# Performance work log

Measured on AMD Instinct MI355X. Metric: run time of the kernel, lower is better.

## Reference

```python
import jax, jax.numpy as jnp
import numpy as np

H = 128        # hidden_channels
NU = 200000    # num users
NM = 80000     # num movies
E = 2_000_000  # num 'rates' edges
EL = 500_000   # num supervision (edge_label) edges
FD = 512       # movie_feat_dim


def setup_inputs() -> dict:
    key = jax.random.key(0)
    ks = jax.random.split(key, 24)
    def w(k, shape):
        # Glorot-ish init for linear weights
        scale = 1.0 / np.sqrt(shape[0])
        return jax.random.uniform(k, shape, jnp.float32, -scale, scale)
    inp = {
        "movie_feats": jax.random.normal(ks[0], (NM, FD), jnp.float32),
        "user_init": jnp.zeros((H,), jnp.float32),  # requires_grad=False param
        "edge_src": jax.random.randint(ks[1], (E,), 0, NU),   # user index per rates-edge
        "edge_dst": jax.random.randint(ks[2], (E,), 0, NM),   # movie index per rates-edge
        "lbl_user": jax.random.randint(ks[3], (EL,), 0, NU),
        "lbl_movie": jax.random.randint(ks[4], (EL,), 0, NM),
        "n_users": NU,
        # movie_lin
        "Wm": w(ks[5], (FD, H)), "bm": jnp.zeros((H,), jnp.float32),
        # conv1, relation user->movie ('rates'): lin_l (neighbor, with bias), lin_r (root, no bias)
        "Wl1_um": w(ks[6], (H, H)), "bl1_um": jnp.zeros((H,), jnp.float32), "Wr1_um": w(ks[7], (H, H)),
        # conv1, relation movie->user ('rev_rates')
        "Wl1_mu": w(ks[8], (H, H)), "bl1_mu": jnp.zeros((H,), jnp.float32), "Wr1_mu": w(ks[9], (H, H)),
        # conv2, user->movie
        "Wl2_um": w(ks[10], (H, H)), "bl2_um": jnp.zeros((H,), jnp.float32), "Wr2_um": w(ks[11], (H, H)),
        # conv2, movie->user
        "Wl2_mu": w(ks[12], (H, H)), "bl2_mu": jnp.zeros((H,), jnp.float32), "Wr2_mu": w(ks[13], (H, H)),
    }
    return inp


def _mean_agg(x_src, src, dst, num_dst):
    # gather source features along edges, scatter-mean into destination nodes
    msgs = x_src[src]                                             # [E, H]
    s = jax.ops.segment_sum(msgs, dst, num_segments=num_dst)      # [num_dst, H]
    cnt = jax.ops.segment_sum(jnp.ones(src.shape, x_src.dtype), dst, num_segments=num_dst)
    return s / jnp.maximum(cnt, 1.0)[:, None]


def _sage(x_src, x_dst, src, dst, Wl, bl, Wr):
    # PyG SAGEConv (aggr='mean'): lin_l(mean_j x_j) + lin_r(x_i); bias only on lin_l
    agg = _mean_agg(x_src, src, dst, x_dst.shape[0])
    return agg @ Wl + bl + x_dst @ Wr


def reference(movie_feats, user_init, edge_src, edge_dst, lbl_user, lbl_movie, n_users,
              Wm, bm,
              Wl1_um, bl1_um, Wr1_um, Wl1_mu, bl1_mu, Wr1_mu,
              Wl2_um, bl2_um, Wr2_um, Wl2_mu, bl2_mu, Wr2_mu):
    # initial node embeddings
    user_x = jnp.tile(user_init[None, :], (n_users, 1))           # [NU, H]
    movie_x = movie_feats @ Wm + bm                               # [NM, H]

    # conv1 (hetero): movie aggregates users via 'rates', user aggregates movies via reverse
    movie_h = _sage(user_x, movie_x, edge_src, edge_dst, Wl1_um, bl1_um, Wr1_um)
    user_h = _sage(movie_x, user_x, edge_dst, edge_src, Wl1_mu, bl1_mu, Wr1_mu)
    movie_h = jax.nn.relu(movie_h)   # dropout p=0.0 -> identity
    user_h = jax.nn.relu(user_h)

    # conv2
    movie_o = _sage(user_h, movie_h, edge_src, edge_dst, Wl2_um, bl2_um, Wr2_um)
    user_o = _sage(movie_h, user_h, edge_dst, edge_src, Wl2_mu, bl2_mu, Wr2_mu)

    # edge-wise dot product on supervision edges
    return (user_o[lbl_user] * movie_o[lbl_movie]).sum(axis=-1)   # [EL]
```

## Files before the change

### kernel.cpp

```cpp
#include <hip/hip_runtime.h>

#define H 128
#define SU 36
#define SM 64

typedef unsigned short u16;
typedef __attribute__((ext_vector_type(8))) short s16x8;
typedef __attribute__((ext_vector_type(4))) float f32x4;

static __device__ __forceinline__ float4 f4zero() { return make_float4(0.f, 0.f, 0.f, 0.f); }
static __device__ __forceinline__ void f4add(float4& a, const float4& b) {
  a.x += b.x; a.y += b.y; a.z += b.z; a.w += b.w;
}
static __device__ __forceinline__ float bf2f(u16 v) {
  return __uint_as_float(((unsigned int)v) << 16);
}
static __device__ __forceinline__ u16 f2bf(float f) {
  unsigned int u = __float_as_uint(f);
  return (u16)((u + 0x7FFF + ((u >> 16) & 1)) >> 16);
}
static __device__ __forceinline__ float4 load4(const u16* p) {
  ushort4 v = *(const ushort4*)p;
  return make_float4(bf2f(v.x), bf2f(v.y), bf2f(v.z), bf2f(v.w));
}
static __device__ __forceinline__ void store4(u16* p, float4 v) {
  ushort4 o;
  o.x = f2bf(v.x); o.y = f2bf(v.y); o.z = f2bf(v.z); o.w = f2bf(v.w);
  *(ushort4*)p = o;
}
static __device__ __forceinline__ void store1(u16* p, float v) { *p = f2bf(v); }

static __device__ __forceinline__ s16x8 frag_from(const u16* p, float) {
  return __builtin_bit_cast(s16x8, *(const uint4*)p);
}
static __device__ __forceinline__ s16x8 frag_from(const float* p, float s) {
  float4 a = *(const float4*)p;
  float4 b = *(const float4*)(p + 4);
  s16x8 v;
  v[0] = (short)f2bf(a.x * s); v[1] = (short)f2bf(a.y * s);
  v[2] = (short)f2bf(a.z * s); v[3] = (short)f2bf(a.w * s);
  v[4] = (short)f2bf(b.x * s); v[5] = (short)f2bf(b.y * s);
  v[6] = (short)f2bf(b.z * s); v[7] = (short)f2bf(b.w * s);
  return v;
}
static __device__ __forceinline__ f32x4 mfma16(s16x8 a, s16x8 b, f32x4 c) {
  return __builtin_amdgcn_mfma_f32_16x16x32_bf16(a, b, c, 0, 0, 0);
}

__global__ void fillfs_u(const int* __restrict__ src, const int* __restrict__ dst,
                         int* __restrict__ cnt, int* __restrict__ adj,
                         float inv, int rbase, int E) {
  int r = (blockIdx.x & 7) + rbase;
  int e = (blockIdx.x >> 3) * blockDim.x + threadIdx.x;
  if (e >= E) return;
  int s = __builtin_nontemporal_load(&src[e]);
  int reg = (int)((float)s * inv);
  if (reg > 15) reg = 15;
  if (reg != r) return;
  int d = __builtin_nontemporal_load(&dst[e]);
  int slot = atomicAdd(&cnt[s], 1);
  if (slot < SU) adj[(size_t)s * SU + slot] = d;
}

__global__ void fillfs_m(const int* __restrict__ src, const int* __restrict__ dst,
                         int* __restrict__ cnt, int* __restrict__ adj,
                         float inv, int E) {
  int r = blockIdx.x & 7;
  int e = (blockIdx.x >> 3) * blockDim.x + threadIdx.x;
  if (e >= E) return;
  int d = __builtin_nontemporal_load(&dst[e]);
  int reg = (int)((float)d * inv);
  if (reg > 7) reg = 7;
  if (reg != r) return;
  int s = __builtin_nontemporal_load(&src[e]);
  int slot = atomicAdd(&cnt[d], 1);
  if (slot < SM) adj[(size_t)d * SM + slot] = s;
}

__global__ void uvec_kernel(const float* __restrict__ u, const float* __restrict__ W1,
                            const float* __restrict__ W2, float* __restrict__ outv1,
                            float* __restrict__ outv2) {
  int h = threadIdx.x;
  float a1 = 0.f, a2 = 0.f;
  for (int k = 0; k < H; k++) {
    float uk = u[k];
    a1 += uk * W1[k * H + h];
    a2 += uk * W2[k * H + h];
  }
  outv1[h] = a1;
  outv2[h] = a2;
}

__global__ void pack_w_all(const float* __restrict__ Wm, const float* __restrict__ Wa,
                           const float* __restrict__ Wb, const float* __restrict__ Wc,
                           const float* __restrict__ Wd, const float* __restrict__ We,
                           const float* __restrict__ Wf, u16* __restrict__ out) {
  int gid = blockIdx.x * blockDim.x + threadIdx.x;
  int chunk = gid >> 11;
  int e = gid & 2047;
  const float* W;
  int kbase = 0;
  if (chunk < 4) { W = Wm; kbase = chunk * 128; }
  else if (chunk == 4) W = Wa;
  else if (chunk == 5) W = Wb;
  else if (chunk == 6) W = Wc;
  else if (chunk == 7) W = Wd;
  else if (chunk == 8) W = We;
  else W = Wf;
  int lane = e & 63;
  int k0 = kbase + ((e >> 6) & 3) * 32 + (lane >> 4) * 8;
  int n = (e >> 8) * 16 + (lane & 15);
  u16 tmp[8];
#pragma unroll
  for (int j = 0; j < 8; j++) tmp[j] = f2bf(W[(size_t)(k0 + j) * H + n]);
  *(uint4*)(out + (size_t)gid * 8) = *(const uint4*)tmp;
}

template <typename TXb>
__global__ __launch_bounds__(256, 4) void mfma_gemm(
    u16* __restrict__ out,
    const u16* __restrict__ Xa, const u16* __restrict__ WpA,
    const TXb* __restrict__ Xb, const u16* __restrict__ WpB, int Kb,
    const float* __restrict__ bl, const float* __restrict__ vec,
    const int* __restrict__ cnt_ind, int relu, int N) {
  int tid = threadIdx.x;
  int lane = tid & 63;
  int wv = tid >> 6;
  int m16 = lane & 15;
  int quad = lane >> 4;
  int rowW = blockIdx.x * 128 + wv * 32;

  f32x4 acc[2][8];
#pragma unroll
  for (int rt = 0; rt < 2; rt++)
#pragma unroll
    for (int ct = 0; ct < 8; ct++) acc[rt][ct] = (f32x4){0.f, 0.f, 0.f, 0.f};

  int ra0 = rowW + m16;      if (ra0 > N - 1) ra0 = N - 1;
  int ra1 = rowW + 16 + m16; if (ra1 > N - 1) ra1 = N - 1;

  if (Xa) {
    const u16* wp = WpA + (size_t)lane * 8;
#pragma unroll
    for (int ks4 = 0; ks4 < 4; ks4++) {
      int ko = ks4 * 32 + quad * 8;
      s16x8 a0 = frag_from(Xa + (size_t)ra0 * 128 + ko, 1.f);
      s16x8 a1 = frag_from(Xa + (size_t)ra1 * 128 + ko, 1.f);
#pragma unroll
      for (int ct = 0; ct < 8; ct++) {
        s16x8 b = __builtin_bit_cast(
            s16x8, *(const uint4*)(wp + ct * 2048 + ks4 * 512));
        acc[0][ct] = mfma16(a0, b, acc[0][ct]);
        acc[1][ct] = mfma16(a1, b, acc[1][ct]);
      }
    }
  }

  if (Xb) {
    for (int kc = 0; kc < Kb; kc += 128) {
      const u16* wp = WpB + (size_t)(kc >> 7) * 16384 + (size_t)lane * 8;
#pragma unroll
      for (int ks4 = 0; ks4 < 4; ks4++) {
        int ko = ks4 * 32 + quad * 8;
        s16x8 a0 = frag_from(Xb + (size_t)ra0 * Kb + kc + ko, 1.f);
        s16x8 a1 = frag_from(Xb + (size_t)ra1 * Kb + kc + ko, 1.f);
#pragma unroll
        for (int ct = 0; ct < 8; ct++) {
          s16x8 b = __builtin_bit_cast(
              s16x8, *(const uint4*)(wp + ct * 2048 + ks4 * 512));
          acc[0][ct] = mfma16(a0, b, acc[0][ct]);
          acc[1][ct] = mfma16(a1, b, acc[1][ct]);
        }
      }
    }
  }

  float bcol[8], vcol[8];
#pragma unroll
  for (int ct = 0; ct < 8; ct++) {
    int col = ct * 16 + m16;
    bcol[ct] = bl ? bl[col] : 0.f;
    vcol[ct] = vec ? vec[col] : 0.f;
  }
#pragma unroll
  for (int rt = 0; rt < 2; rt++) {
#pragma unroll
    for (int rg = 0; rg < 4; rg++) {
      int r = rowW + rt * 16 + quad * 4 + rg;
      if (r >= N) continue;
      float ind = 0.f;
      if (vec) ind = (cnt_ind ? (cnt_ind[r] > 0 ? 1.f : 0.f) : 1.f);
#pragma unroll
      for (int ct = 0; ct < 8; ct++) {
        float o = acc[rt][ct][rg] + bcol[ct] + ind * vcol[ct];
        if (relu) o = fmaxf(o, 0.f);
        store1(out + (size_t)r * H + ct * 16 + m16, o);
      }
    }
  }
}

__global__ __launch_bounds__(256) void agg_bf(
    u16* __restrict__ outb, const u16* __restrict__ xsrc,
    const int* __restrict__ adj, int stride,
    const int* __restrict__ cnt, const float* __restrict__ bl,
    const float* __restrict__ vec, int mode, int N) {
  int wid = (blockIdx.x * blockDim.x + threadIdx.x) >> 6;
  if (wid >= N) return;
  int lane = threadIdx.x & 63;
  int c4 = lane & 31;
  int slot = lane >> 5;
  size_t s0 = (size_t)wid * stride;
  int c = cnt[wid];
  int cl = c > stride ? stride : c;
  float4 acc = f4zero();
  int i = slot;
  while (i + 6 < cl) {
    int n0 = adj[s0 + i];
    int n1 = adj[s0 + i + 2];
    int n2 = adj[s0 + i + 4];
    int n3 = adj[s0 + i + 6];
    float4 v0 = load4(xsrc + (size_t)n0 * H + c4 * 4);
    float4 v1 = load4(xsrc + (size_t)n1 * H + c4 * 4);
    float4 v2 = load4(xsrc + (size_t)n2 * H + c4 * 4);
    float4 v3 = load4(xsrc + (size_t)n3 * H + c4 * 4);
    f4add(acc, v0);
    f4add(acc, v1);
    f4add(acc, v2);
    f4add(acc, v3);
    i += 8;
  }
  while (i < cl) {
    int n0 = adj[s0 + i];
    float4 v0 = load4(xsrc + (size_t)n0 * H + c4 * 4);
    f4add(acc, v0);
    i += 2;
  }
  acc.x += __shfl_xor(acc.x, 32);
  acc.y += __shfl_xor(acc.y, 32);
  acc.z += __shfl_xor(acc.z, 32);
  acc.w += __shfl_xor(acc.w, 32);
  if (slot == 0) {
    float s = 1.f / (float)(c > 1 ? c : 1);
    u16* op = outb + (size_t)wid * H + c4 * 4;
    if (mode == 1) {
      float4 o = load4(op);
      o.x += s * acc.x; o.y += s * acc.y; o.z += s * acc.z; o.w += s * acc.w;
      store4(op, o);
    } else if (mode == 2) {
      float4 b4 = *(const float4*)(bl + c4 * 4);
      float4 r4 = *(const float4*)(vec + c4 * 4);
      float4 o;
      o.x = fmaxf(s * acc.x + b4.x + r4.x, 0.f);
      o.y = fmaxf(s * acc.y + b4.y + r4.y, 0.f);
      o.z = fmaxf(s * acc.z + b4.z + r4.z, 0.f);
      o.w = fmaxf(s * acc.w + b4.w + r4.w, 0.f);
      store4(op, o);
    } else {
      float4 o;
      o.x = s * acc.x; o.y = s * acc.y; o.z = s * acc.z; o.w = s * acc.w;
      store4(op, o);
    }
  }
}

__global__ void dot_bf(float* __restrict__ outp, const u16* __restrict__ U,
                       const u16* __restrict__ M, const int* __restrict__ lu,
                       const int* __restrict__ lm, int EL) {
  int g = blockIdx.x * blockDim.x + threadIdx.x;
  int e = g >> 5;
  int l = g & 31;
  if (e >= EL) return;
  float4 a = load4(U + (size_t)lu[e] * H + l * 4);
  float4 b = load4(M + (size_t)lm[e] * H + l * 4);
  float p = a.x * b.x + a.y * b.y + a.z * b.z + a.w * b.w;
#pragma unroll
  for (int off = 16; off > 0; off >>= 1) p += __shfl_xor(p, off);
  if (l == 0) outp[e] = p;
}

extern "C" void kernel_launch(void* const* d_in, const int* in_sizes, int n_in,
                              void* d_out, int out_size, void* d_ws, size_t ws_size,
                              hipStream_t stream) {
  const float* movie_feats = (const float*)d_in[0];
  const float* user_init = (const float*)d_in[1];
  const int* edge_src = (const int*)d_in[2];
  const int* edge_dst = (const int*)d_in[3];
  const int* lbl_user = (const int*)d_in[4];
  const int* lbl_movie = (const int*)d_in[5];
  const float* Wm = (const float*)d_in[7];
  const float* bm = (const float*)d_in[8];
  const float* Wl1_um = (const float*)d_in[9];
  const float* bl1_um = (const float*)d_in[10];
  const float* Wr1_um = (const float*)d_in[11];
  const float* Wl1_mu = (const float*)d_in[12];
  const float* bl1_mu = (const float*)d_in[13];
  const float* Wr1_mu = (const float*)d_in[14];
  const float* Wl2_um = (const float*)d_in[15];
  const float* bl2_um = (const float*)d_in[16];
  const float* Wr2_um = (const float*)d_in[17];
  const float* Wl2_mu = (const float*)d_in[18];
  const float* bl2_mu = (const float*)d_in[19];
  const float* Wr2_mu = (const float*)d_in[20];

  const int FD = 512;
  const int NU = 200000;
  const int NM = in_sizes[0] / FD;
  const int E = in_sizes[2];
  const int EL = in_sizes[4];

  char* w = (char*)d_ws;
  auto carve = [&](size_t bytes) {
    char* p = w;
    w += (bytes + 255) & ~(size_t)255;
    return p;
  };
  u16* A16 = (u16*)carve((size_t)NM * H * 2);
  u16* B16 = (u16*)carve((size_t)NU * H * 2);
  u16* D16 = (u16*)carve((size_t)NM * H * 2);
  u16* M16 = (u16*)carve((size_t)NM * H * 2);
  u16* UO16 = (u16*)carve((size_t)NU * H * 2);
  int* cnt_u = (int*)carve((size_t)NU * 4);
  int* cnt_m = (int*)carve((size_t)NM * 4);
  int* adj_u = (int*)carve((size_t)NU * SU * 4);
  float* r1vec = (float*)carve(512);
  float* l1vec = (float*)carve(512);
  u16* Wp = (u16*)carve((size_t)10 * 16384 * 2);
  int* adj_m = (int*)UO16;
  u16* G16 = A16;
  u16* AU16 = A16;

  hipMemsetAsync(cnt_u, 0, (size_t)NU * 4, stream);
  hipMemsetAsync(cnt_m, 0, (size_t)NM * 4, stream);

  const int tb = 256;
  pack_w_all<<<80, tb, 0, stream>>>(Wm, Wl1_mu, Wr1_um, Wl2_um, Wr2_um, Wl2_mu,
                                    Wr2_mu, Wp);
  u16* WpWm = Wp;
  u16* Wp1mu = Wp + 4 * 16384;
  u16* Wp1um = Wp + 5 * 16384;
  u16* Wp2lum = Wp + 6 * 16384;
  u16* Wp2rum = Wp + 7 * 16384;
  u16* Wp2lmu = Wp + 8 * 16384;
  u16* Wp2rmu = Wp + 9 * 16384;

  int nchunk = (E + tb - 1) / tb;
  fillfs_u<<<nchunk * 8, tb, 0, stream>>>(edge_src, edge_dst, cnt_u, adj_u,
                                          16.0f / (float)NU, 0, E);
  fillfs_u<<<nchunk * 8, tb, 0, stream>>>(edge_src, edge_dst, cnt_u, adj_u,
                                          16.0f / (float)NU, 8, E);
  fillfs_m<<<nchunk * 8, tb, 0, stream>>>(edge_src, edge_dst, cnt_m, adj_m,
                                          8.0f / (float)NM, E);

  uvec_kernel<<<1, H, 0, stream>>>(user_init, Wr1_mu, Wl1_um, r1vec, l1vec);

  int gNM = NM / 128;
  int gNU = (NU + 127) / 128;

  mfma_gemm<float><<<gNM, tb, 0, stream>>>(
      A16, nullptr, nullptr, movie_feats, WpWm, FD, bm, nullptr, nullptr, 0, NM);
  mfma_gemm<u16><<<gNM, tb, 0, stream>>>(
      D16, nullptr, nullptr, A16, Wp1mu, H, nullptr, nullptr, nullptr, 0, NM);
  agg_bf<<<((size_t)NU * 64 + tb - 1) / tb, tb, 0, stream>>>(
      B16, D16, adj_u, SU, cnt_u, bl1_mu, r1vec, 2, NU);
  mfma_gemm<u16><<<gNM, tb, 0, stream>>>(
      M16, nullptr, nullptr, A16, Wp1um, H, bl1_um, l1vec, cnt_m, 1, NM);
  agg_bf<<<((size_t)NM * 64 + tb - 1) / tb, tb, 0, stream>>>(
      G16, B16, adj_m, SM, cnt_m, nullptr, nullptr, 3, NM);
  mfma_gemm<u16><<<gNM, tb, 0, stream>>>(
      D16, G16, Wp2lum, M16, Wp2rum, H, bl2_um, nullptr, nullptr, 0, NM);
  mfma_gemm<u16><<<gNM, tb, 0, stream>>>(
      AU16, nullptr, nullptr, M16, Wp2lmu, H, nullptr, nullptr, nullptr, 0, NM);
  mfma_gemm<u16><<<gNU, tb, 0, stream>>>(
      UO16, nullptr, nullptr, B16, Wp2rmu, H, bl2_mu, nullptr, nullptr, 0, NU);
  agg_bf<<<((size_t)NU * 64 + tb - 1) / tb, tb, 0, stream>>>(
      UO16, AU16, adj_u, SU, cnt_u, nullptr, nullptr, 1, NU);
  dot_bf<<<((size_t)EL * 32 + tb - 1) / tb, tb, 0, stream>>>((float*)d_out, UO16, D16,
                                                             lbl_user, lbl_movie, EL);
}
```

Before: 1.018 ms.

## Fuse both user-side aggregations into one pass and widen gather loads

Reorders the pipeline so the conv2 movie->user projection is computed before the first user aggregation. A single agg2 kernel can then gather both the conv1 and conv2 movie tables over the user adjacency in one pass, and the final user GEMM folds in the aggregated term through a new addin input. Aggregation and dot kernels switch to 16-byte bf16 loads with 8 values per lane, and adjacency indices use nontemporal loads. adj_m gets its own workspace buffer instead of aliasing UO16, which adds memory use; the shared gather reads twice the bytes per edge but drops a full pass over adj_u.

Result: faster. 955.3 us (-6.1%).

```diff
diff --git a/kernel.cpp b/kernel.cpp
--- a/kernel.cpp
+++ b/kernel.cpp
@@ -8,10 +8,6 @@
 typedef __attribute__((ext_vector_type(8))) short s16x8;
 typedef __attribute__((ext_vector_type(4))) float f32x4;
 
-static __device__ __forceinline__ float4 f4zero() { return make_float4(0.f, 0.f, 0.f, 0.f); }
-static __device__ __forceinline__ void f4add(float4& a, const float4& b) {
-  a.x += b.x; a.y += b.y; a.z += b.z; a.w += b.w;
-}
 static __device__ __forceinline__ float bf2f(u16 v) {
   return __uint_as_float(((unsigned int)v) << 16);
 }
@@ -19,16 +15,18 @@
   unsigned int u = __float_as_uint(f);
   return (u16)((u + 0x7FFF + ((u >> 16) & 1)) >> 16);
 }
-static __device__ __forceinline__ float4 load4(const u16* p) {
-  ushort4 v = *(const ushort4*)p;
-  return make_float4(bf2f(v.x), bf2f(v.y), bf2f(v.z), bf2f(v.w));
-}
-static __device__ __forceinline__ void store4(u16* p, float4 v) {
-  ushort4 o;
-  o.x = f2bf(v.x); o.y = f2bf(v.y); o.z = f2bf(v.z); o.w = f2bf(v.w);
-  *(ushort4*)p = o;
-}
 static __device__ __forceinline__ void store1(u16* p, float v) { *p = f2bf(v); }
+
+static __device__ __forceinline__ void acc8(float* a, uint4 v) {
+  a[0] += __uint_as_float(v.x << 16);
+  a[1] += __uint_as_float(v.x & 0xffff0000u);
+  a[2] += __uint_as_float(v.y << 16);
+  a[3] += __uint_as_float(v.y & 0xffff0000u);
+  a[4] += __uint_as_float(v.z << 16);
+  a[5] += __uint_as_float(v.z & 0xffff0000u);
+  a[6] += __uint_as_float(v.w << 16);
+  a[7] += __uint_as_float(v.w & 0xffff0000u);
+}
 
 static __device__ __forceinline__ s16x8 frag_from(const u16* p, float) {
   return __builtin_bit_cast(s16x8, *(const uint4*)p);
@@ -122,7 +120,8 @@
     const u16* __restrict__ Xa, const u16* __restrict__ WpA,
     const TXb* __restrict__ Xb, const u16* __restrict__ WpB, int Kb,
     const float* __restrict__ bl, const float* __restrict__ vec,
-    const int* __restrict__ cnt_ind, int relu, int N) {
+    const int* __restrict__ cnt_ind, const u16* __restrict__ addin,
+    int relu, int N) {
   int tid = threadIdx.x;
   int lane = tid & 63;
   int wv = tid >> 6;
@@ -193,6 +192,7 @@
 #pragma unroll
       for (int ct = 0; ct < 8; ct++) {
         float o = acc[rt][ct][rg] + bcol[ct] + ind * vcol[ct];
+        if (addin) o += bf2f(addin[(size_t)r * H + ct * 16 + m16]);
         if (relu) o = fmaxf(o, 0.f);
         store1(out + (size_t)r * H + ct * 16 + m16, o);
       }
@@ -200,67 +200,108 @@
   }
 }
 
-__global__ __launch_bounds__(256) void agg_bf(
-    u16* __restrict__ outb, const u16* __restrict__ xsrc,
-    const int* __restrict__ adj, int stride,
-    const int* __restrict__ cnt, const float* __restrict__ bl,
-    const float* __restrict__ vec, int mode, int N) {
+__global__ __launch_bounds__(256) void agg2_bf(
+    u16* __restrict__ outB, u16* __restrict__ outS,
+    const u16* __restrict__ TD, const u16* __restrict__ TA,
+    const int* __restrict__ adj, int stride, const int* __restrict__ cnt,
+    const float* __restrict__ bl, const float* __restrict__ vec, int N) {
   int wid = (blockIdx.x * blockDim.x + threadIdx.x) >> 6;
   if (wid >= N) return;
   int lane = threadIdx.x & 63;
-  int c4 = lane & 31;
-  int slot = lane >> 5;
+  int c16 = lane & 15;
+  int slot = lane >> 4;
   size_t s0 = (size_t)wid * stride;
   int c = cnt[wid];
   int cl = c > stride ? stride : c;
-  float4 acc = f4zero();
+  float aD[8] = {0.f, 0.f, 0.f, 0.f, 0.f, 0.f, 0.f, 0.f};
+  float aA[8] = {0.f, 0.f, 0.f, 0.f, 0.f, 0.f, 0.f, 0.f};
+  int co = c16 * 8;
   int i = slot;
-  while (i + 6 < cl) {
-    int n0 = adj[s0 + i];
-    int n1 = adj[s0 + i + 2];
-    int n2 = adj[s0 + i + 4];
-    int n3 = adj[s0 + i + 6];
-    float4 v0 = load4(xsrc + (size_t)n0 * H + c4 * 4);
-    float4 v1 = load4(xsrc + (size_t)n1 * H + c4 * 4);
-    float4 v2 = load4(xsrc + (size_t)n2 * H + c4 * 4);
-    float4 v3 = load4(xsrc + (size_t)n3 * H + c4 * 4);
-    f4add(acc, v0);
-    f4add(acc, v1);
-    f4add(acc, v2);
-    f4add(acc, v3);
+  while (i + 4 < cl) {
+    int n0 = __builtin_nontemporal_load(&adj[s0 + i]);
+    int n1 = __builtin_nontemporal_load(&adj[s0 + i + 4]);
+    uint4 d0 = *(const uint4*)(TD + (size_t)n0 * H + co);
+    uint4 a0 = *(const uint4*)(TA + (size_t)n0 * H + co);
+    uint4 d1 = *(const uint4*)(TD + (size_t)n1 * H + co);
+    uint4 a1 = *(const uint4*)(TA + (size_t)n1 * H + co);
+    acc8(aD, d0); acc8(aD, d1); acc8(aA, a0); acc8(aA, a1);
     i += 8;
   }
   while (i < cl) {
-    int n0 = adj[s0 + i];
-    float4 v0 = load4(xsrc + (size_t)n0 * H + c4 * 4);
-    f4add(acc, v0);
-    i += 2;
-  }
-  acc.x += __shfl_xor(acc.x, 32);
-  acc.y += __shfl_xor(acc.y, 32);
-  acc.z += __shfl_xor(acc.z, 32);
-  acc.w += __shfl_xor(acc.w, 32);
+    int n0 = __builtin_nontemporal_load(&adj[s0 + i]);
+    uint4 d0 = *(const uint4*)(TD + (size_t)n0 * H + co);
+    uint4 a0 = *(const uint4*)(TA + (size_t)n0 * H + co);
+    acc8(aD, d0); acc8(aA, a0);
+    i += 4;
+  }
+#pragma unroll
+  for (int j = 0; j < 8; j++) {
+    aD[j] += __shfl_xor(aD[j], 16); aD[j] += __shfl_xor(aD[j], 32);
+    aA[j] += __shfl_xor(aA[j], 16); aA[j] += __shfl_xor(aA[j], 32);
+  }
   if (slot == 0) {
     float s = 1.f / (float)(c > 1 ? c : 1);
-    u16* op = outb + (size_t)wid * H + c4 * 4;
-    if (mode == 1) {
-      float4 o = load4(op);
-      o.x += s * acc.x; o.y += s * acc.y; o.z += s * acc.z; o.w += s * acc.w;
-      store4(op, o);
-    } else if (mode == 2) {
-      float4 b4 = *(const float4*)(bl + c4 * 4);
-      float4 r4 = *(const float4*)(vec + c4 * 4);
-      float4 o;
-      o.x = fmaxf(s * acc.x + b4.x + r4.x, 0.f);
-      o.y = fmaxf(s * acc.y + b4.y + r4.y, 0.f);
-      o.z = fmaxf(s * acc.z + b4.z + r4.z, 0.f);
-      o.w = fmaxf(s * acc.w + b4.w + r4.w, 0.f);
-      store4(op, o);
-    } else {
-      float4 o;
-      o.x = s * acc.x; o.y = s * acc.y; o.z = s * acc.z; o.w = s * acc.w;
-      store4(op, o);
+    u16 ob[8], os[8];
+#pragma unroll
+    for (int j = 0; j < 8; j++) {
+      ob[j] = f2bf(fmaxf(s * aD[j] + bl[co + j] + vec[co + j], 0.f));
+      os[j] = f2bf(s * aA[j]);
     }
+    *(uint4*)(outB + (size_t)wid * H + co) = *(const uint4*)ob;
+    *(uint4*)(outS + (size_t)wid * H + co) = *(const uint4*)os;
+  }
+}
+
+__global__ __launch_bounds__(256) void agg1_bf(
+    u16* __restrict__ out, const u16* __restrict__ T,
+    const int* __restrict__ adj, int stride, const int* __restrict__ cnt, int N) {
+  int wid = (blockIdx.x * blockDim.x + threadIdx.x) >> 6;
+  if (wid >= N) return;
+  int lane = threadIdx.x & 63;
+  int c16 = lane & 15;
+  int slot = lane >> 4;
+  size_t s0 = (size_t)wid * stride;
+  int c = cnt[wid];
+  int cl = c > stride ? stride : c;
+  float a[8] = {0.f, 0.f, 0.f, 0.f, 0.f, 0.f, 0.f, 0.f};
+  int co = c16 * 8;
+  int i = slot;
+  while (i + 12 < cl) {
+    int n0 = __builtin_nontemporal_load(&adj[s0 + i]);
+    int n1 = __builtin_nontemporal_load(&adj[s0 + i + 4]);
+    int n2 = __builtin_nontemporal_load(&adj[s0 + i + 8]);
+    int n3 = __builtin_nontemporal_load(&adj[s0 + i + 12]);
+    uint4 v0 = *(const uint4*)(T + (size_t)n0 * H + co);
+    uint4 v1 = *(const uint4*)(T + (size_t)n1 * H + co);
+    uint4 v2 = *(const uint4*)(T + (size_t)n2 * H + co);
+    uint4 v3 = *(const uint4*)(T + (size_t)n3 * H + co);
+    acc8(a, v0); acc8(a, v1); acc8(a, v2); acc8(a, v3);
+    i += 16;
+  }
+  while (i + 4 < cl) {
+    int n0 = __builtin_nontemporal_load(&adj[s0 + i]);
+    int n1 = __builtin_nontemporal_load(&adj[s0 + i + 4]);
+    uint4 v0 = *(const uint4*)(T + (size_t)n0 * H + co);
+    uint4 v1 = *(const uint4*)(T + (size_t)n1 * H + co);
+    acc8(a, v0); acc8(a, v1);
+    i += 8;
+  }
+  while (i < cl) {
+    int n0 = __builtin_nontemporal_load(&adj[s0 + i]);
+    uint4 v0 = *(const uint4*)(T + (size_t)n0 * H + co);
+    acc8(a, v0);
+    i += 4;
+  }
+#pragma unroll
+  for (int j = 0; j < 8; j++) {
+    a[j] += __shfl_xor(a[j], 16); a[j] += __shfl_xor(a[j], 32);
+  }
+  if (slot == 0) {
+    float s = 1.f / (float)(c > 1 ? c : 1);
+    u16 o[8];
+#pragma unroll
+    for (int j = 0; j < 8; j++) o[j] = f2bf(s * a[j]);
+    *(uint4*)(out + (size_t)wid * H + co) = *(const uint4*)o;
   }
 }
 
@@ -268,14 +309,22 @@
                        const u16* __restrict__ M, const int* __restrict__ lu,
                        const int* __restrict__ lm, int EL) {
   int g = blockIdx.x * blockDim.x + threadIdx.x;
-  int e = g >> 5;
-  int l = g & 31;
+  int e = g >> 4;
+  int l = g & 15;
   if (e >= EL) return;
-  float4 a = load4(U + (size_t)lu[e] * H + l * 4);
-  float4 b = load4(M + (size_t)lm[e] * H + l * 4);
-  float p = a.x * b.x + a.y * b.y + a.z * b.z + a.w * b.w;
-#pragma unroll
-  for (int off = 16; off > 0; off >>= 1) p += __shfl_xor(p, off);
+  uint4 a = *(const uint4*)(U + (size_t)lu[e] * H + l * 8);
+  uint4 b = *(const uint4*)(M + (size_t)lm[e] * H + l * 8);
+  float p = 0.f;
+  p += __uint_as_float(a.x << 16) * __uint_as_float(b.x << 16);
+  p += __uint_as_float(a.x & 0xffff0000u) * __uint_as_float(b.x & 0xffff0000u);
+  p += __uint_as_float(a.y << 16) * __uint_as_float(b.y << 16);
+  p += __uint_as_float(a.y & 0xffff0000u) * __uint_as_float(b.y & 0xffff0000u);
+  p += __uint_as_float(a.z << 16) * __uint_as_float(b.z << 16);
+  p += __uint_as_float(a.z & 0xffff0000u) * __uint_as_float(b.z & 0xffff0000u);
+  p += __uint_as_float(a.w << 16) * __uint_as_float(b.w << 16);
+  p += __uint_as_float(a.w & 0xffff0000u) * __uint_as_float(b.w & 0xffff0000u);
+#pragma unroll
+  for (int off = 8; off > 0; off >>= 1) p += __shfl_xor(p, off);
   if (l == 0) outp[e] = p;
 }
 
@@ -323,12 +372,12 @@
   int* cnt_u = (int*)carve((size_t)NU * 4);
   int* cnt_m = (int*)carve((size_t)NM * 4);
   int* adj_u = (int*)carve((size_t)NU * SU * 4);
+  int* adj_m = (int*)carve((size_t)NM * SM * 4);
   float* r1vec = (float*)carve(512);
   float* l1vec = (float*)carve(512);
   u16* Wp = (u16*)carve((size_t)10 * 16384 * 2);
-  int* adj_m = (int*)UO16;
+  u16* AU16 = A16;
   u16* G16 = A16;
-  u16* AU16 = A16;
 
   hipMemsetAsync(cnt_u, 0, (size_t)NU * 4, stream);
   hipMemsetAsync(cnt_m, 0, (size_t)NM * 4, stream);
@@ -358,23 +407,27 @@
   int gNU = (NU + 127) / 128;
 
   mfma_gemm<float><<<gNM, tb, 0, stream>>>(
-      A16, nullptr, nullptr, movie_feats, WpWm, FD, bm, nullptr, nullptr, 0, NM);
+      A16, nullptr, nullptr, movie_feats, WpWm, FD, bm, nullptr, nullptr,
+      nullptr, 0, NM);
   mfma_gemm<u16><<<gNM, tb, 0, stream>>>(
-      D16, nullptr, nullptr, A16, Wp1mu, H, nullptr, nullptr, nullptr, 0, NM);
-  agg_bf<<<((size_t)NU * 64 + tb - 1) / tb, tb, 0, stream>>>(
-      B16, D16, adj_u, SU, cnt_u, bl1_mu, r1vec, 2, NU);
+      D16, nullptr, nullptr, A16, Wp1mu, H, nullptr, nullptr, nullptr,
+      nullptr, 0, NM);
   mfma_gemm<u16><<<gNM, tb, 0, stream>>>(
-      M16, nullptr, nullptr, A16, Wp1um, H, bl1_um, l1vec, cnt_m, 1, NM);
-  agg_bf<<<((size_t)NM * 64 + tb - 1) / tb, tb, 0, stream>>>(
-      G16, B16, adj_m, SM, cnt_m, nullptr, nullptr, 3, NM);
+      M16, nullptr, nullptr, A16, Wp1um, H, bl1_um, l1vec, cnt_m,
+      nullptr, 1, NM);
   mfma_gemm<u16><<<gNM, tb, 0, stream>>>(
-      D16, G16, Wp2lum, M16, Wp2rum, H, bl2_um, nullptr, nullptr, 0, NM);
+      AU16, nullptr, nullptr, M16, Wp2lmu, H, nullptr, nullptr, nullptr,
+      nullptr, 0, NM);
+  agg2_bf<<<((size_t)NU * 64 + tb - 1) / tb, tb, 0, stream>>>(
+      B16, UO16, D16, AU16, adj_u, SU, cnt_u, bl1_mu, r1vec, NU);
+  agg1_bf<<<((size_t)NM * 64 + tb - 1) / tb, tb, 0, stream>>>(
+      G16, B16, adj_m, SM, cnt_m, NM);
   mfma_gemm<u16><<<gNM, tb, 0, stream>>>(
-      AU16, nullptr, nullptr, M16, Wp2lmu, H, nullptr, nullptr, nullptr, 0, NM);
+      D16, G16, Wp2lum, M16, Wp2rum, H, bl2_um, nullptr, nullptr,
+      nullptr, 0, NM);
   mfma_gemm<u16><<<gNU, tb, 0, stream>>>(
-      UO16, nullptr, nullptr, B16, Wp2rmu, H, bl2_mu, nullptr, nullptr, 0, NU);
-  agg_bf<<<((size_t)NU * 64 + tb - 1) / tb, tb, 0, stream>>>(
-      UO16, AU16, adj_u, SU, cnt_u, nullptr, nullptr, 1, NU);
-  dot_bf<<<((size_t)EL * 32 + tb - 1) / tb, tb, 0, stream>>>((float*)d_out, UO16, D16,
+      UO16, nullptr, nullptr, B16, Wp2rmu, H, bl2_mu, nullptr, nullptr,
+      UO16, 0, NU);
+  dot_bf<<<((size_t)EL * 16 + tb - 1) / tb, tb, 0, stream>>>((float*)d_out, UO16, D16,
                                                              lbl_user, lbl_movie, EL);
 }
```
